# Kernel tuning notes

Measured on AMD Instinct MI355X. Metric: run time of the kernel, lower is better.

## Reference

```python
import jax, jax.numpy as jnp
import numpy as np


def mha(x, mask, wq, bq, wk, bk, wv, bv, wo, bo, n_heads):
    # Flaubert/XLM MultiHeadAttention (eval mode, dropout = identity).
    bs, qlen, dim = x.shape
    dph = dim // n_heads

    def split_heads(t):  # (bs, qlen, dim) -> (bs, n_heads, qlen, dph)
        return t.reshape(bs, qlen, n_heads, dph).transpose(0, 2, 1, 3)

    q = split_heads(x @ wq + bq) / jnp.sqrt(jnp.asarray(dph, x.dtype))
    k = split_heads(x @ wk + bk)
    v = split_heads(x @ wv + bv)

    scores = jnp.einsum('bhqd,bhkd->bhqk', q, k)  # (bs, h, qlen, klen)
    neg = jnp.finfo(scores.dtype).min
    scores = jnp.where((mask == 0)[:, None, None, :], neg, scores)
    weights = jax.nn.softmax(scores, axis=-1)
    ctx = jnp.einsum('bhqk,bhkd->bhqd', weights, v)
    ctx = ctx.transpose(0, 2, 1, 3).reshape(bs, qlen, dim)
    return ctx @ wo + bo


def setup_inputs() -> dict:
    key = jax.random.key(0)
    ks = jax.random.split(key, 20)
    bs, slen = 4, 1024
    d0, d1 = 192, 66
    std = 0.02
    inp = {
        'x': jax.random.normal(ks[0], (bs, slen, d0), jnp.float32),
        'y': jax.random.normal(ks[1], (bs, slen, d1), jnp.float32),
        'mask0': jax.random.randint(ks[2], (bs, slen), 0, 2, jnp.int32),
        'mask1': jax.random.randint(ks[3], (bs, slen), 0, 2, jnp.int32),
    }
    names0 = ['q0', 'k0', 'v0', 'o0']
    names1 = ['q1', 'k1', 'v1', 'o1']
    for i, n in enumerate(names0):
        inp[n + '_w'] = jax.random.normal(ks[4 + i], (d0, d0), jnp.float32) * std
        inp[n + '_b'] = jnp.zeros((d0,), jnp.float32)
    for i, n in enumerate(names1):
        inp[n + '_w'] = jax.random.normal(ks[8 + i], (d1, d1), jnp.float32) * std
        inp[n + '_b'] = jnp.zeros((d1,), jnp.float32)
    return inp


def reference(x, y, mask0, mask1,
              q0_w, q0_b, k0_w, k0_b, v0_w, v0_b, o0_w, o0_b,
              q1_w, q1_b, k1_w, k1_b, v1_w, v1_b, o1_w, o1_b):
    out0 = mha(x, mask0, q0_w, q0_b, k0_w, k0_b, v0_w, v0_b, o0_w, o0_b, n_heads=16)
    out1 = mha(y, mask1, q1_w, q1_b, k1_w, k1_b, v1_w, v1_b, o1_w, o1_b, n_heads=11)
    return (out0, out1)
```

## Files before the change

kernel.cpp:

```cpp
#include <hip/hip_runtime.h>
#include <math.h>


#define BS 4
#define SLEN 1024

#define Q0_OFF 0
#define C0_OFF 786432
#define Q1_OFF 1572864
#define C1_OFF 1843200
#define K0H_OFF 2113536
#define V0T_OFF 2506752
#define K1H_OFF 2899968
#define V1T_OFF 3080192
#define CMAP0_OFF 3215360
#define CMAP1_OFF 3219456
#define CNT_OFF 3223552

#define OUT0_SIZE 786432

#if __has_builtin(__builtin_amdgcn_exp2f)
#define EXP2(x) __builtin_amdgcn_exp2f(x)
#else
#define EXP2(x) __expf((x) * 0.69314718056f)
#endif

typedef _Float16 f16x2 __attribute__((ext_vector_type(2)));
typedef _Float16 f16x4 __attribute__((ext_vector_type(4)));
typedef _Float16 f16x8 __attribute__((ext_vector_type(8)));
typedef float f32x4 __attribute__((ext_vector_type(4)));

union F16x8U { f16x8 v8; f16x4 v4[2]; };

__global__ __launch_bounds__(256) void compact_kernel(
    const int* __restrict__ mask0, const int* __restrict__ mask1,
    int* __restrict__ cmap0, int* __restrict__ cmap1, int* __restrict__ cnts)
{
  __shared__ int sS[256];
  __shared__ int sTot;
  const int inst = blockIdx.x >> 2, b = blockIdx.x & 3;
  const int* m = (inst ? mask1 : mask0) + b * SLEN;
  int* cmap = (inst ? cmap1 : cmap0) + b * SLEN;
  const int tid = threadIdx.x;

  int mv[4], s4 = 0;
#pragma unroll
  for (int i = 0; i < 4; ++i) { mv[i] = m[tid * 4 + i] ? 1 : 0; s4 += mv[i]; }
  sS[tid] = s4;
  __syncthreads();
  for (int off = 1; off < 256; off <<= 1) {
    const int v = sS[tid];
    const int add = (tid >= off) ? sS[tid - off] : 0;
    __syncthreads();
    sS[tid] = v + add;
    __syncthreads();
  }
  if (tid == 255) sTot = sS[255];
  __syncthreads();
  const int tot = sTot;
  int u = tid ? sS[tid - 1] : 0;
#pragma unroll
  for (int i = 0; i < 4; ++i) {
    const int s = tid * 4 + i;
    cmap[s] = mv[i] ? u : tot + (s - u);
    u += mv[i];
  }
  if (tid == 0) cnts[blockIdx.x] = tot;
}

__device__ __forceinline__ void mfma_chunk(const _Float16* sA, const _Float16* sWT,
                                           int wv, int lane, f32x4 acc[4])
{
  const int col = lane & 15, grp = lane >> 4;
#pragma unroll
  for (int ks = 0; ks < 2; ++ks) {
    const f16x8 bf = *(const f16x8*)(sWT + (wv * 16 + col) * 72 + ks * 32 + grp * 8);
#pragma unroll
    for (int mt = 0; mt < 4; ++mt) {
      const f16x8 af = *(const f16x8*)(sA + (mt * 16 + col) * 72 + ks * 32 + grp * 8);
      acc[mt] = __builtin_amdgcn_mfma_f32_16x16x32_f16(af, bf, acc[mt], 0, 0, 0);
    }
  }
}

__device__ __forceinline__ void mfma_chunk_split(
    const _Float16* sAh, const _Float16* sAl,
    const _Float16* sWTh, const _Float16* sWTl,
    int wv, int lane, f32x4 acc[4])
{
  const int col = lane & 15, grp = lane >> 4;
#pragma unroll
  for (int ks = 0; ks < 2; ++ks) {
    const int boff = (wv * 16 + col) * 72 + ks * 32 + grp * 8;
    const f16x8 bh = *(const f16x8*)(sWTh + boff);
    const f16x8 bl = *(const f16x8*)(sWTl + boff);
#pragma unroll
    for (int mt = 0; mt < 4; ++mt) {
      const int aoff = (mt * 16 + col) * 72 + ks * 32 + grp * 8;
      const f16x8 ah = *(const f16x8*)(sAh + aoff);
      const f16x8 al = *(const f16x8*)(sAl + aoff);
      acc[mt] = __builtin_amdgcn_mfma_f32_16x16x32_f16(ah, bh, acc[mt], 0, 0, 0);
      acc[mt] = __builtin_amdgcn_mfma_f32_16x16x32_f16(ah, bl, acc[mt], 0, 0, 0);
      acc[mt] = __builtin_amdgcn_mfma_f32_16x16x32_f16(al, bh, acc[mt], 0, 0, 0);
    }
  }
}

template <int DIM>
__device__ __forceinline__ void stage_chunk(const float* __restrict__ A, int row0,
                                            int kc, const float* __restrict__ W,
                                            int col0, _Float16* sA, _Float16* sWT,
                                            int tid)
{
  for (int idx = tid; idx < 2048; idx += 256) {
    const int m = idx >> 5, k = (idx & 31) * 2;
    float2 v = make_float2(0.f, 0.f);
    if (kc + k < DIM) v = *(const float2*)(A + (size_t)(row0 + m) * DIM + kc + k);
    *(f16x2*)(sA + m * 72 + k) = (f16x2){(_Float16)v.x, (_Float16)v.y};
  }
  for (int idx = tid; idx < 2048; idx += 256) {
    const int k = idx >> 5, n = (idx & 31) * 2;
    float2 v = make_float2(0.f, 0.f);
    if (kc + k < DIM && col0 + n < DIM)
      v = *(const float2*)(W + (size_t)(kc + k) * DIM + col0 + n);
    sWT[n * 72 + k] = (_Float16)v.x;
    sWT[(n + 1) * 72 + k] = (_Float16)v.y;
  }
}

template <int DIM>
__device__ __forceinline__ void stage_chunk_split(
    const float* __restrict__ A, int row0, int kc,
    const float* __restrict__ W, int col0,
    _Float16* sAh, _Float16* sAl, _Float16* sWTh, _Float16* sWTl, int tid)
{
  for (int idx = tid; idx < 2048; idx += 256) {
    const int m = idx >> 5, k = (idx & 31) * 2;
    float2 v = make_float2(0.f, 0.f);
    if (kc + k < DIM) v = *(const float2*)(A + (size_t)(row0 + m) * DIM + kc + k);
    const _Float16 hx = (_Float16)v.x, hy = (_Float16)v.y;
    *(f16x2*)(sAh + m * 72 + k) = (f16x2){hx, hy};
    *(f16x2*)(sAl + m * 72 + k) =
        (f16x2){(_Float16)(v.x - (float)hx), (_Float16)(v.y - (float)hy)};
  }
  for (int idx = tid; idx < 2048; idx += 256) {
    const int k = idx >> 5, n = (idx & 31) * 2;
    float2 v = make_float2(0.f, 0.f);
    if (kc + k < DIM && col0 + n < DIM)
      v = *(const float2*)(W + (size_t)(kc + k) * DIM + col0 + n);
    const _Float16 hx = (_Float16)v.x, hy = (_Float16)v.y;
    sWTh[n * 72 + k] = hx;
    sWTh[(n + 1) * 72 + k] = hy;
    sWTl[n * 72 + k] = (_Float16)(v.x - (float)hx);
    sWTl[(n + 1) * 72 + k] = (_Float16)(v.y - (float)hy);
  }
}

template <int DIM, int H, int DPH, int NT, int NCH, int KST>
__device__ void qkv_impl(int bid, const float* __restrict__ X,
                         const float* __restrict__ qw, const float* __restrict__ qb,
                         const float* __restrict__ kw, const float* __restrict__ kb,
                         const float* __restrict__ vw, const float* __restrict__ vb,
                         float* __restrict__ qo, _Float16* __restrict__ kh,
                         _Float16* __restrict__ vth, const int* __restrict__ cmap,
                         char* smem)
{
  const int mt64 = bid & 63;
  const int rest = bid >> 6;
  const int mat = rest / NT;
  const int nt = rest % NT;
  const int row0 = mt64 * 64, col0 = nt * 64;

  const float* W = (mat == 0) ? qw : (mat == 1) ? kw : vw;
  const float* B = (mat == 0) ? qb : (mat == 1) ? kb : vb;
  const float scale = (mat == 0) ? (1.44269504089f / sqrtf((float)DPH)) : 1.0f;

  _Float16* sA = (_Float16*)smem;
  _Float16* sWT = sA + 64 * 72;

  const int tid = threadIdx.x;
  const int wv = tid >> 6, lane = tid & 63;
  f32x4 acc[4] = {{0.f,0.f,0.f,0.f},{0.f,0.f,0.f,0.f},{0.f,0.f,0.f,0.f},{0.f,0.f,0.f,0.f}};

  for (int c = 0; c < NCH; ++c) {
    __syncthreads();
    stage_chunk<DIM>(X, row0, c * 64, W, col0, sA, sWT, tid);
    __syncthreads();
    mfma_chunk(sA, sWT, wv, lane, acc);
  }

  const int col = lane & 15, grp = lane >> 4;
  const int cidx = col0 + wv * 16 + col;
  if (cidx < DIM) {
    const float bias = B[cidx];
    const int h = cidx / DPH, d = cidx % DPH;
#pragma unroll
    for (int mt = 0; mt < 4; ++mt) {
#pragma unroll
      for (int r = 0; r < 4; ++r) {
        const int m = row0 + mt * 16 + grp * 4 + r;
        const int b = m >> 10, s = m & 1023;
        const float v = acc[mt][r] + bias;
        const int bh = b * H + h;
        if (mat == 0) {
          qo[(size_t)((bh << 10) + s) * DPH + d] = v * scale;
        } else {
          const int sp = cmap[(b << 10) + s];
          if (mat == 1)
            kh[(size_t)((bh << 10) + sp) * KST + d] = (_Float16)v;
          else
            vth[((size_t)(bh * DPH + d) << 10) + sp] = (_Float16)v;
        }
      }
    }
  }
}

__global__ __launch_bounds__(256) void qkv_kernel(
    const float* __restrict__ x, const float* __restrict__ y,
    const float* __restrict__ q0w, const float* __restrict__ q0b,
    const float* __restrict__ k0w, const float* __restrict__ k0b,
    const float* __restrict__ v0w, const float* __restrict__ v0b,
    const float* __restrict__ q1w, const float* __restrict__ q1b,
    const float* __restrict__ k1w, const float* __restrict__ k1b,
    const float* __restrict__ v1w, const float* __restrict__ v1b,
    float* __restrict__ ws)
{
  extern __shared__ char smem[];
  _Float16* hws = (_Float16*)ws;
  const int* cmap0 = (const int*)(ws + CMAP0_OFF);
  const int* cmap1 = (const int*)(ws + CMAP1_OFF);
  const int bid = blockIdx.x;
  if (bid < 576)
    qkv_impl<192, 16, 12, 3, 3, 12>(bid, x, q0w, q0b, k0w, k0b, v0w, v0b,
                                    ws + Q0_OFF, hws + 2 * (size_t)K0H_OFF,
                                    hws + 2 * (size_t)V0T_OFF, cmap0, smem);
  else
    qkv_impl<66, 11, 6, 2, 2, 8>(bid - 576, y, q1w, q1b, k1w, k1b, v1w, v1b,
                                 ws + Q1_OFF, hws + 2 * (size_t)K1H_OFF,
                                 hws + 2 * (size_t)V1T_OFF, cmap1, smem);
}

template <int H, int DPH, int SKP>
__device__ void attn_impl(int bid, const float* __restrict__ qg,
                          const _Float16* __restrict__ kh,
                          const _Float16* __restrict__ vth,
                          const int* __restrict__ cnts,
                          float* __restrict__ ctx, char* smem)
{
  constexpr int CH = 128;
  constexpr int NKC = CH / 32;
  constexpr int KBUF = CH * SKP + 32;
  constexpr int VST = 136;
  constexpr int VROWS = DPH + 1;
  constexpr int PST = 44;
  constexpr int PWAVE = 16 * PST;

  _Float16* sK = (_Float16*)smem;
  _Float16* sVT = sK + 2 * KBUF;
  _Float16* sP = sVT + 2 * VROWS * VST;

  const int bh = bid >> 4;
  const int b = bh / H;
  const int h = bh % H;
  const int tid = threadIdx.x;

  const float* qb_ = qg + (size_t)bh * SLEN * DPH;
  const _Float16* kb_ = kh + (size_t)bh * SLEN * SKP;
  const _Float16* vb_ = vth + ((size_t)bh * DPH << 10);
  const int cnt = cnts[b];
  const int nch = (cnt + CH - 1) >> 7;

  if (tid < 64) sK[(tid >> 5) * KBUF + CH * SKP + (tid & 31)] = (_Float16)0.f;
  for (int idx = tid; idx < 2 * CH; idx += 256) {
    const int pb = idx / CH, q = idx % CH;
    sVT[(pb * VROWS + DPH) * VST + q] = (_Float16)1.f;
  }

  const int wave = tid >> 6, lane = tid & 63;
  const int col = lane & 15, grp = lane >> 4;
  const int qtile = (bid & 15) * 4 + wave;

  f16x8 aq;
  {
    const int qrow = qtile * 16 + col;
#pragma unroll
    for (int j = 0; j < 8; ++j) {
      const int d = grp * 8 + j;
      aq[j] = (d < DPH) ? (_Float16)qb_[(size_t)qrow * DPH + d] : (_Float16)0.f;
    }
  }

  constexpr int kN = CH * SKP / 8;
  constexpr int vN = DPH * 16;
  const int vd = tid >> 4, vq = tid & 15;
  uint4 pk, pv;
  auto prefetch = [&](int cc) {
    if (tid < kN) pk = ((const uint4*)(kb_ + (size_t)cc * CH * SKP))[tid];
    if (tid < vN) pv = ((const uint4*)(vb_ + ((size_t)vd << 10) + cc * CH))[vq];
  };
  auto commit = [&](int pb) {
    if (tid < kN) ((uint4*)(sK + pb * KBUF))[tid] = pk;
    if (tid < vN) *(uint4*)(sVT + (pb * VROWS + vd) * VST + vq * 8) = pv;
  };

  prefetch(0);
  commit(0);
  __syncthreads();

  f32x4 Oacc[2] = {{0.f,0.f,0.f,0.f},{0.f,0.f,0.f,0.f}};
  const int de = (col <= DPH) ? col : 0;

#pragma unroll 1
  for (int c = 0; c < nch; ++c) {
    const int p = c & 1;
    if (c + 1 < nch) prefetch(c + 1);

    const _Float16* sKp = sK + p * KBUF;
    const _Float16* sVp = sVT + p * VROWS * VST;
    const int keyc = c * CH + col;

    f32x4 S0, S1;
    {
      F16x8U kf0, kf1;
      const _Float16* kp0 = sKp + col * SKP + grp * 8;
      const _Float16* kp1 = sKp + (16 + col) * SKP + grp * 8;
      kf0.v4[0] = *(const f16x4*)kp0; kf0.v4[1] = *(const f16x4*)(kp0 + 4);
      kf1.v4[0] = *(const f16x4*)kp1; kf1.v4[1] = *(const f16x4*)(kp1 + 4);
      const float bb0 = (keyc < cnt) ? 0.f : -100.f;
      const float bb1 = (keyc + 16 < cnt) ? 0.f : -100.f;
      S0 = __builtin_amdgcn_mfma_f32_16x16x32_f16(
          aq, kf0.v8, (f32x4){bb0, bb0, bb0, bb0}, 0, 0, 0);
      S1 = __builtin_amdgcn_mfma_f32_16x16x32_f16(
          aq, kf1.v8, (f32x4){bb1, bb1, bb1, bb1}, 0, 0, 0);
    }

#pragma unroll
    for (int kc = 0; kc < NKC; ++kc) {
      f32x4 S0n, S1n;
      if (kc + 1 < NKC) {
        F16x8U kf0, kf1;
        const _Float16* kp0 = sKp + ((kc + 1) * 32 + col) * SKP + grp * 8;
        const _Float16* kp1 = sKp + ((kc + 1) * 32 + 16 + col) * SKP + grp * 8;
        kf0.v4[0] = *(const f16x4*)kp0; kf0.v4[1] = *(const f16x4*)(kp0 + 4);
        kf1.v4[0] = *(const f16x4*)kp1; kf1.v4[1] = *(const f16x4*)(kp1 + 4);
        const float bb0 = (keyc + (kc + 1) * 32 < cnt) ? 0.f : -100.f;
        const float bb1 = (keyc + (kc + 1) * 32 + 16 < cnt) ? 0.f : -100.f;
        S0n = __builtin_amdgcn_mfma_f32_16x16x32_f16(
            aq, kf0.v8, (f32x4){bb0, bb0, bb0, bb0}, 0, 0, 0);
        S1n = __builtin_amdgcn_mfma_f32_16x16x32_f16(
            aq, kf1.v8, (f32x4){bb1, bb1, bb1, bb1}, 0, 0, 0);
      }

      _Float16* pw = sP + (wave * 2 + (kc & 1)) * PWAVE + col;
#pragma unroll
      for (int r = 0; r < 4; ++r) {
        pw[(grp * 4 + r) * PST] = (_Float16)EXP2(S0[r]);
        pw[(grp * 4 + r) * PST + 16] = (_Float16)EXP2(S1[r]);
      }

      if (kc > 0) {
        const f16x8 vf = *(const f16x8*)(sVp + de * VST + (kc - 1) * 32 + grp * 8);
        F16x8U pf;
        const _Float16* pr =
            sP + (wave * 2 + ((kc - 1) & 1)) * PWAVE + col * PST + grp * 8;
        pf.v4[0] = *(const f16x4*)pr;
        pf.v4[1] = *(const f16x4*)(pr + 4);
        Oacc[(kc - 1) & 1] = __builtin_amdgcn_mfma_f32_16x16x32_f16(
            pf.v8, vf, Oacc[(kc - 1) & 1], 0, 0, 0);
      }
      S0 = S0n; S1 = S1n;
    }

    {
      constexpr int kl = NKC - 1;
      const f16x8 vf = *(const f16x8*)(sVp + de * VST + kl * 32 + grp * 8);
      F16x8U pf;
      const _Float16* pr =
          sP + (wave * 2 + (kl & 1)) * PWAVE + col * PST + grp * 8;
      pf.v4[0] = *(const f16x4*)pr;
      pf.v4[1] = *(const f16x4*)(pr + 4);
      Oacc[kl & 1] = __builtin_amdgcn_mfma_f32_16x16x32_f16(
          pf.v8, vf, Oacc[kl & 1], 0, 0, 0);
    }

    if (c + 1 < nch) commit(p ^ 1);
    __syncthreads();
  }

  f32x4 Osum;
#pragma unroll
  for (int r = 0; r < 4; ++r) Osum[r] = Oacc[0][r] + Oacc[1][r];
  float lq[4];
#pragma unroll
  for (int r = 0; r < 4; ++r) lq[r] = __shfl(Osum[r], (lane & 48) + DPH);
  if (col < DPH) {
    const int qrow0 = qtile * 16;
#pragma unroll
    for (int r = 0; r < 4; ++r) {
      const int row = qrow0 + grp * 4 + r;
      ctx[(size_t)(b * SLEN + row) * (H * DPH) + h * DPH + col] = Osum[r] / lq[r];
    }
  }
}

__global__ __launch_bounds__(256) void attn_kernel(float* __restrict__ ws)
{
  extern __shared__ char smem[];
  _Float16* hws = (_Float16*)ws;
  const int* cnts = (const int*)(ws + CNT_OFF);
  const int bid = blockIdx.x;
  if (bid < 1024)
    attn_impl<16, 12, 12>(bid, ws + Q0_OFF, hws + 2 * (size_t)K0H_OFF,
                          hws + 2 * (size_t)V0T_OFF, cnts, ws + C0_OFF, smem);
  else
    attn_impl<11, 6, 8>(bid - 1024, ws + Q1_OFF, hws + 2 * (size_t)K1H_OFF,
                        hws + 2 * (size_t)V1T_OFF, cnts + 4, ws + C1_OFF, smem);
}

template <int DIM, int NCH>
__device__ void oproj_impl(int bid, const float* __restrict__ Cx,
                           const float* __restrict__ ow, const float* __restrict__ ob,
                           float* __restrict__ out, char* smem)
{
  const int mt64 = bid & 63;
  const int nt = bid >> 6;
  const int row0 = mt64 * 64, col0 = nt * 64;

  _Float16* sAh = (_Float16*)smem;
  _Float16* sAl = sAh + 64 * 72;
  _Float16* sWTh = sAl + 64 * 72;
  _Float16* sWTl = sWTh + 64 * 72;

  const int tid = threadIdx.x;
  const int wv = tid >> 6, lane = tid & 63;
  f32x4 acc[4] = {{0.f,0.f,0.f,0.f},{0.f,0.f,0.f,0.f},{0.f,0.f,0.f,0.f},{0.f,0.f,0.f,0.f}};

  for (int c = 0; c < NCH; ++c) {
    __syncthreads();
    stage_chunk_split<DIM>(Cx, row0, c * 64, ow, col0, sAh, sAl, sWTh, sWTl, tid);
    __syncthreads();
    mfma_chunk_split(sAh, sAl, sWTh, sWTl, wv, lane, acc);
  }

  const int col = lane & 15, grp = lane >> 4;
  const int cidx = col0 + wv * 16 + col;
  if (cidx < DIM) {
    const float bias = ob[cidx];
#pragma unroll
    for (int mt = 0; mt < 4; ++mt) {
#pragma unroll
      for (int r = 0; r < 4; ++r) {
        const int m = row0 + mt * 16 + grp * 4 + r;
        out[(size_t)m * DIM + cidx] = acc[mt][r] + bias;
      }
    }
  }
}

__global__ __launch_bounds__(256) void oproj_kernel(
    const float* __restrict__ o0w, const float* __restrict__ o0b,
    const float* __restrict__ o1w, const float* __restrict__ o1b,
    float* __restrict__ ws, float* __restrict__ out)
{
  extern __shared__ char smem[];
  const int bid = blockIdx.x;
  if (bid < 192)
    oproj_impl<192, 3>(bid, ws + C0_OFF, o0w, o0b, out, smem);
  else
    oproj_impl<66, 2>(bid - 192, ws + C1_OFF, o1w, o1b, out + OUT0_SIZE, smem);
}

extern "C" void kernel_launch(void* const* d_in, const int* in_sizes, int n_in,
                              void* d_out, int out_size, void* d_ws, size_t ws_size,
                              hipStream_t stream)
{
  const float* x = (const float*)d_in[0];
  const float* y = (const float*)d_in[1];
  const int* mask0 = (const int*)d_in[2];
  const int* mask1 = (const int*)d_in[3];
  const float* q0w = (const float*)d_in[4];  const float* q0b = (const float*)d_in[5];
  const float* k0w = (const float*)d_in[6];  const float* k0b = (const float*)d_in[7];
  const float* v0w = (const float*)d_in[8];  const float* v0b = (const float*)d_in[9];
  const float* o0w = (const float*)d_in[10]; const float* o0b = (const float*)d_in[11];
  const float* q1w = (const float*)d_in[12]; const float* q1b = (const float*)d_in[13];
  const float* k1w = (const float*)d_in[14]; const float* k1b = (const float*)d_in[15];
  const float* v1w = (const float*)d_in[16]; const float* v1b = (const float*)d_in[17];
  const float* o1w = (const float*)d_in[18]; const float* o1b = (const float*)d_in[19];

  float* ws = (float*)d_ws;
  float* out = (float*)d_out;

  const int qkv_smem = 2 * 64 * 72 * 2;
  const int oproj_smem = 4 * 64 * 72 * 2;
  const int attn_smem = 2 * (128 * 12 + 32) * 2 + 2 * 13 * 136 * 2
                      + 4 * 2 * (16 * 44) * 2;

  compact_kernel<<<8, 256, 0, stream>>>(mask0, mask1,
                                        (int*)(ws + CMAP0_OFF),
                                        (int*)(ws + CMAP1_OFF),
                                        (int*)(ws + CNT_OFF));
  qkv_kernel<<<960, 256, qkv_smem, stream>>>(x, y, q0w, q0b, k0w, k0b, v0w, v0b,
                                             q1w, q1b, k1w, k1b, v1w, v1b, ws);
  attn_kernel<<<1728, 256, attn_smem, stream>>>(ws);
  oproj_kernel<<<320, 256, oproj_smem, stream>>>(o0w, o0b, o1w, o1b, ws, out);
}
```

Baseline: 158.3 us.

## Keep attention probabilities in registers using transposed 16x16x16 MFMA chain

The attention inner loop switches from 16x16x32 MFMAs with a shared-memory round trip for P to 16x16x16 MFMAs that compute S^T, so the exp'd scores already sit in the A-operand layout for the PV MFMA. This removes the sP scratch buffer, its LDS stores and loads, and the ones-row trick in V^T used for the row sum. The row sum is now accumulated in registers and reduced with cross-lane shuffles. The trade-off is twice as many smaller MFMAs and a K dimension padded only to 16, plus extra exp and sum work per lane.

```diff
diff --git a/kernel.cpp b/kernel.cpp
--- a/kernel.cpp
+++ b/kernel.cpp
@@ -249,16 +249,11 @@
                           float* __restrict__ ctx, char* smem)
 {
   constexpr int CH = 128;
-  constexpr int NKC = CH / 32;
   constexpr int KBUF = CH * SKP + 32;
   constexpr int VST = 136;
-  constexpr int VROWS = DPH + 1;
-  constexpr int PST = 44;
-  constexpr int PWAVE = 16 * PST;
 
   _Float16* sK = (_Float16*)smem;
   _Float16* sVT = sK + 2 * KBUF;
-  _Float16* sP = sVT + 2 * VROWS * VST;
 
   const int bh = bid >> 4;
   const int b = bh / H;
@@ -272,21 +267,17 @@
   const int nch = (cnt + CH - 1) >> 7;
 
   if (tid < 64) sK[(tid >> 5) * KBUF + CH * SKP + (tid & 31)] = (_Float16)0.f;
-  for (int idx = tid; idx < 2 * CH; idx += 256) {
-    const int pb = idx / CH, q = idx % CH;
-    sVT[(pb * VROWS + DPH) * VST + q] = (_Float16)1.f;
-  }
 
   const int wave = tid >> 6, lane = tid & 63;
   const int col = lane & 15, grp = lane >> 4;
   const int qtile = (bid & 15) * 4 + wave;
 
-  f16x8 aq;
+  f16x4 aq;
   {
     const int qrow = qtile * 16 + col;
 #pragma unroll
-    for (int j = 0; j < 8; ++j) {
-      const int d = grp * 8 + j;
+    for (int j = 0; j < 4; ++j) {
+      const int d = grp * 4 + j;
       aq[j] = (d < DPH) ? (_Float16)qb_[(size_t)qrow * DPH + d] : (_Float16)0.f;
     }
   }
@@ -301,7 +292,7 @@
   };
   auto commit = [&](int pb) {
     if (tid < kN) ((uint4*)(sK + pb * KBUF))[tid] = pk;
-    if (tid < vN) *(uint4*)(sVT + (pb * VROWS + vd) * VST + vq * 8) = pv;
+    if (tid < vN) *(uint4*)(sVT + (pb * DPH + vd) * VST + vq * 8) = pv;
   };
 
   prefetch(0);
@@ -309,7 +300,8 @@
   __syncthreads();
 
   f32x4 Oacc[2] = {{0.f,0.f,0.f,0.f},{0.f,0.f,0.f,0.f}};
-  const int de = (col <= DPH) ? col : 0;
+  float lsum = 0.f;
+  const int de = (col < DPH) ? col : 0;
 
 #pragma unroll 1
   for (int c = 0; c < nch; ++c) {
@@ -317,71 +309,26 @@
     if (c + 1 < nch) prefetch(c + 1);
 
     const _Float16* sKp = sK + p * KBUF;
-    const _Float16* sVp = sVT + p * VROWS * VST;
-    const int keyc = c * CH + col;
-
-    f32x4 S0, S1;
-    {
-      F16x8U kf0, kf1;
-      const _Float16* kp0 = sKp + col * SKP + grp * 8;
-      const _Float16* kp1 = sKp + (16 + col) * SKP + grp * 8;
-      kf0.v4[0] = *(const f16x4*)kp0; kf0.v4[1] = *(const f16x4*)(kp0 + 4);
-      kf1.v4[0] = *(const f16x4*)kp1; kf1.v4[1] = *(const f16x4*)(kp1 + 4);
-      const float bb0 = (keyc < cnt) ? 0.f : -100.f;
-      const float bb1 = (keyc + 16 < cnt) ? 0.f : -100.f;
-      S0 = __builtin_amdgcn_mfma_f32_16x16x32_f16(
-          aq, kf0.v8, (f32x4){bb0, bb0, bb0, bb0}, 0, 0, 0);
-      S1 = __builtin_amdgcn_mfma_f32_16x16x32_f16(
-          aq, kf1.v8, (f32x4){bb1, bb1, bb1, bb1}, 0, 0, 0);
-    }
-
-#pragma unroll
-    for (int kc = 0; kc < NKC; ++kc) {
-      f32x4 S0n, S1n;
-      if (kc + 1 < NKC) {
-        F16x8U kf0, kf1;
-        const _Float16* kp0 = sKp + ((kc + 1) * 32 + col) * SKP + grp * 8;
-        const _Float16* kp1 = sKp + ((kc + 1) * 32 + 16 + col) * SKP + grp * 8;
-        kf0.v4[0] = *(const f16x4*)kp0; kf0.v4[1] = *(const f16x4*)(kp0 + 4);
-        kf1.v4[0] = *(const f16x4*)kp1; kf1.v4[1] = *(const f16x4*)(kp1 + 4);
-        const float bb0 = (keyc + (kc + 1) * 32 < cnt) ? 0.f : -100.f;
-        const float bb1 = (keyc + (kc + 1) * 32 + 16 < cnt) ? 0.f : -100.f;
-        S0n = __builtin_amdgcn_mfma_f32_16x16x32_f16(
-            aq, kf0.v8, (f32x4){bb0, bb0, bb0, bb0}, 0, 0, 0);
-        S1n = __builtin_amdgcn_mfma_f32_16x16x32_f16(
-            aq, kf1.v8, (f32x4){bb1, bb1, bb1, bb1}, 0, 0, 0);
-      }
-
-      _Float16* pw = sP + (wave * 2 + (kc & 1)) * PWAVE + col;
-#pragma unroll
-      for (int r = 0; r < 4; ++r) {
-        pw[(grp * 4 + r) * PST] = (_Float16)EXP2(S0[r]);
-        pw[(grp * 4 + r) * PST + 16] = (_Float16)EXP2(S1[r]);
-      }
-
-      if (kc > 0) {
-        const f16x8 vf = *(const f16x8*)(sVp + de * VST + (kc - 1) * 32 + grp * 8);
-        F16x8U pf;
-        const _Float16* pr =
-            sP + (wave * 2 + ((kc - 1) & 1)) * PWAVE + col * PST + grp * 8;
-        pf.v4[0] = *(const f16x4*)pr;
-        pf.v4[1] = *(const f16x4*)(pr + 4);
-        Oacc[(kc - 1) & 1] = __builtin_amdgcn_mfma_f32_16x16x32_f16(
-            pf.v8, vf, Oacc[(kc - 1) & 1], 0, 0, 0);
-      }
-      S0 = S0n; S1 = S1n;
-    }
-
-    {
-      constexpr int kl = NKC - 1;
-      const f16x8 vf = *(const f16x8*)(sVp + de * VST + kl * 32 + grp * 8);
-      F16x8U pf;
-      const _Float16* pr =
-          sP + (wave * 2 + (kl & 1)) * PWAVE + col * PST + grp * 8;
-      pf.v4[0] = *(const f16x4*)pr;
-      pf.v4[1] = *(const f16x4*)(pr + 4);
-      Oacc[kl & 1] = __builtin_amdgcn_mfma_f32_16x16x32_f16(
-          pf.v8, vf, Oacc[kl & 1], 0, 0, 0);
+    const _Float16* sVp = sVT + p * DPH * VST;
+    const int keyr = c * CH + grp * 4;
+
+#pragma unroll
+    for (int kt = 0; kt < CH / 16; ++kt) {
+      const f16x4 kf = *(const f16x4*)(sKp + (kt * 16 + col) * SKP + grp * 4);
+      const int k0 = keyr + kt * 16;
+      const f32x4 biasv = {(k0 < cnt) ? 0.f : -100.f,
+                           (k0 + 1 < cnt) ? 0.f : -100.f,
+                           (k0 + 2 < cnt) ? 0.f : -100.f,
+                           (k0 + 3 < cnt) ? 0.f : -100.f};
+      const f32x4 S = __builtin_amdgcn_mfma_f32_16x16x16f16(kf, aq, biasv,
+                                                            0, 0, 0);
+      const float e0 = EXP2(S[0]), e1 = EXP2(S[1]);
+      const float e2 = EXP2(S[2]), e3 = EXP2(S[3]);
+      lsum += (e0 + e1) + (e2 + e3);
+      const f16x4 pf = {(_Float16)e0, (_Float16)e1, (_Float16)e2, (_Float16)e3};
+      const f16x4 vf = *(const f16x4*)(sVp + de * VST + kt * 16 + grp * 4);
+      Oacc[kt & 1] = __builtin_amdgcn_mfma_f32_16x16x16f16(pf, vf, Oacc[kt & 1],
+                                                           0, 0, 0);
     }
 
     if (c + 1 < nch) commit(p ^ 1);
@@ -391,9 +338,12 @@
   f32x4 Osum;
 #pragma unroll
   for (int r = 0; r < 4; ++r) Osum[r] = Oacc[0][r] + Oacc[1][r];
+  float lred = lsum;
+  lred += __shfl_xor(lred, 16);
+  lred += __shfl_xor(lred, 32);
   float lq[4];
 #pragma unroll
-  for (int r = 0; r < 4; ++r) lq[r] = __shfl(Osum[r], (lane & 48) + DPH);
+  for (int r = 0; r < 4; ++r) lq[r] = __shfl(lred, grp * 4 + r);
   if (col < DPH) {
     const int qrow0 = qtile * 16;
 #pragma unroll
@@ -493,8 +443,7 @@
 
   const int qkv_smem = 2 * 64 * 72 * 2;
   const int oproj_smem = 4 * 64 * 72 * 2;
-  const int attn_smem = 2 * (128 * 12 + 32) * 2 + 2 * 13 * 136 * 2
-                      + 4 * 2 * (16 * 44) * 2;
+  const int attn_smem = 2 * (128 * 12 + 32) * 2 + 2 * 12 * 136 * 2;
 
   compact_kernel<<<8, 256, 0, stream>>>(mask0, mask1,
                                         (int*)(ws + CMAP0_OFF),
```

Measured after the change: 157.3 us. No clear change (-0.6%).
